# Optimization experiments

Measured on AMD Instinct MI355X. Metric: run time of the kernel, lower is better.

## Reference

```python
import jax, jax.numpy as jnp
import numpy as np

BATCH = 4096
DIM = 2048
TEMPERATURE = 0.5


def setup_inputs() -> dict:
    key = jax.random.key(0)
    k1, k2 = jax.random.split(key)
    c_i = jax.random.normal(k1, (BATCH, DIM), dtype=jnp.float32)
    c_j = jax.random.normal(k2, (BATCH, DIM), dtype=jnp.float32)
    return {"c_i": c_i, "c_j": c_j}


def reference(c_i, c_j):
    # Original torch loop computes, for each i,j:
    #   kl[i, j] = sum_k softmax(c_j[j])_k * (log_softmax(c_j[j])_k - log_softmax(c_i[i])_k)
    #   logits = -kl / T ; loss = CE(logits, arange(B), reduction='sum') / B
    # Fused: kl = hneg[None, :] - Li @ Q.T where hneg[j] = sum_k Q[j]*logQ[j].
    B = c_i.shape[0]
    Li = jax.nn.log_softmax(c_i, axis=-1)          # [B, D]
    LQ = jax.nn.log_softmax(c_j, axis=-1)          # [B, D]
    Q = jnp.exp(LQ)                                # softmax(c_j)
    hneg = jnp.sum(Q * LQ, axis=-1)                # [B] negative entropy of each c_j row
    cross = jnp.einsum("id,jd->ij", Li, Q)         # [B, B] sum_k Li[i,k]*Q[j,k]
    kl = hneg[None, :] - cross                     # [B, B]
    logits = -kl / TEMPERATURE
    logp = jax.nn.log_softmax(logits, axis=-1)     # [B, B]
    loss = -jnp.sum(jnp.diagonal(logp)) / B        # CE(sum) / batch_size
    return loss
```

## Files before the change

kernel.cpp:

```cpp
#include <hip/hip_runtime.h>
#include <hip/hip_bf16.h>
#include <math.h>

#define BATCH 4096
#define DIM   2048
#define INV_T 2.0f

#define BM 256
#define BN 256

typedef float floatx4 __attribute__((ext_vector_type(4)));
typedef int   intx4   __attribute__((ext_vector_type(4)));
typedef int   intx8   __attribute__((ext_vector_type(8)));

static __device__ __forceinline__ void gld_lds16(const void* g, void* l) {
  __builtin_amdgcn_global_load_lds(
      (const __attribute__((address_space(1))) void*)g,
      (__attribute__((address_space(3))) void*)l, 16, 0, 0);
}

static __device__ __forceinline__ intx8 comb8(intx4 lo, intx4 hi) {
  intx8 r;
  r[0] = lo[0]; r[1] = lo[1]; r[2] = lo[2]; r[3] = lo[3];
  r[4] = hi[0]; r[5] = hi[1]; r[6] = hi[2]; r[7] = hi[3];
  return r;
}

__global__ __launch_bounds__(256) void prep_kernel(
    const float* __restrict__ ci, const float* __restrict__ cj,
    unsigned char* __restrict__ Li8, unsigned char* __restrict__ Qb8,
    float* __restrict__ hneg, float* __restrict__ isc,
    float* __restrict__ rowsum, unsigned* __restrict__ cnt)
{
  const int lane = threadIdx.x & 63;
  const int wave = threadIdx.x >> 6;
  const int row = blockIdx.x * 4 + wave;
  const bool isj = row >= BATCH;
  const int r = isj ? row - BATCH : row;
  const float* __restrict__ src = (isj ? cj : ci) + (size_t)r * DIM;

  float v[32];
  #pragma unroll
  for (int i = 0; i < 8; ++i) {
    float4 t = ((const float4*)src)[i * 64 + lane];
    v[i * 4 + 0] = t.x; v[i * 4 + 1] = t.y;
    v[i * 4 + 2] = t.z; v[i * 4 + 3] = t.w;
  }

  float m = v[0];
  #pragma unroll
  for (int i = 1; i < 32; ++i) m = fmaxf(m, v[i]);
  #pragma unroll
  for (int off = 32; off >= 1; off >>= 1) m = fmaxf(m, __shfl_xor(m, off));

  float e[32];
  float s = 0.f;
  #pragma unroll
  for (int i = 0; i < 32; ++i) { e[i] = __expf(v[i] - m); s += e[i]; }
  #pragma unroll
  for (int off = 32; off >= 1; off >>= 1) s += __shfl_xor(s, off);
  const float ls = m + __logf(s);
  const float inv_s = 1.0f / s;

  float scale = 1.f;
  int t = 0;
  if (isj) {
    const int be = (int)((__float_as_uint(inv_s) >> 23) & 0xff);
    t = 134 - be;
    scale = __uint_as_float((unsigned)(t + 127) << 23);
  }

  unsigned char* dst = (isj ? Qb8 : Li8) + (size_t)r * DIM;
  float h = 0.f;
  #pragma unroll
  for (int i = 0; i < 8; ++i) {
    float f[4];
    #pragma unroll
    for (int j = 0; j < 4; ++j) {
      const float li = v[i * 4 + j] - ls;
      if (isj) {
        const float q = e[i * 4 + j] * inv_s;
        h += q * li;
        f[j] = q * scale;
      } else {
        f[j] = li;
      }
    }
    int w = __builtin_amdgcn_cvt_pk_fp8_f32(f[0], f[1], 0, false);
    w = __builtin_amdgcn_cvt_pk_fp8_f32(f[2], f[3], w, true);
    ((int*)dst)[i * 64 + lane] = w;
  }

  if (isj) {
    #pragma unroll
    for (int off = 32; off >= 1; off >>= 1) h += __shfl_xor(h, off);
    if (lane == 0) {
      hneg[r] = h;
      isc[r] = __uint_as_float((unsigned)(127 - t) << 23);
      rowsum[r] = 0.f;
    }
  }
  if (row == 0 && lane == 0) cnt[0] = 0u;
}

__global__ __launch_bounds__(512, 1) void gemm_lse_kernel(
    const unsigned char* __restrict__ Li8, const unsigned char* __restrict__ Qb8,
    const float* __restrict__ hneg, const float* __restrict__ isc,
    float* __restrict__ rowsum, float* __restrict__ diag,
    unsigned* __restrict__ cnt, float* __restrict__ out)
{
  __shared__ __attribute__((aligned(16))) unsigned char As_[2][BM * 128];
  __shared__ __attribute__((aligned(16))) unsigned char Bs_[2][BN * 128];

  const int tid  = threadIdx.x;
  const int lin = blockIdx.x;
  const int xc  = lin & 7;
  const int sq  = lin >> 3;
  const int by  = (xc & 3) * 4 + (sq & 3);
  const int bx  = (xc >> 2) * 8 + (sq >> 2);

  const int lane = tid & 63;
  const int wave = tid >> 6;
  const int wm   = wave >> 2;
  const int wn   = wave & 3;

  int soff[4];
  #pragma unroll
  for (int s = 0; s < 4; ++s) {
    const int p = tid + 512 * s;
    const int row = p >> 3;
    const int cbg = (p & 7) ^ (row & 7);
    soff[s] = row * DIM + cbg * 16;
  }
  const unsigned char* Abase = Li8 + (size_t)(by * BM) * DIM;
  const unsigned char* Bbase = Qb8 + (size_t)(bx * BN) * DIM;

  const int rl = lane & 15;
  const int q  = lane >> 4;
  const int sw = rl & 7;

  floatx4 acc[8][4];
  const floatx4 z = {0.f, 0.f, 0.f, 0.f};
  #pragma unroll
  for (int mt = 0; mt < 8; ++mt)
    #pragma unroll
    for (int nt = 0; nt < 4; ++nt) acc[mt][nt] = z;

  #pragma unroll
  for (int s = 0; s < 4; ++s) {
    gld_lds16(Abase + soff[s], &As_[0][0] + (tid + 512 * s) * 16);
    gld_lds16(Bbase + soff[s], &Bs_[0][0] + (tid + 512 * s) * 16);
  }

  for (int t = 0; t < 16; ++t) {
    const int cur = t & 1;
    const unsigned char* Ab = &As_[cur][0];
    const unsigned char* Bb = &Bs_[cur][0];

    if (t < 15) {
      unsigned char* An = &As_[cur ^ 1][0];
      unsigned char* Bn = &Bs_[cur ^ 1][0];
      const int kn = (t + 1) * 128;
      #pragma unroll
      for (int s = 0; s < 4; ++s) {
        gld_lds16(Abase + soff[s] + kn, An + (tid + 512 * s) * 16);
        gld_lds16(Bbase + soff[s] + kn, Bn + (tid + 512 * s) * 16);
      }
      asm volatile("s_waitcnt vmcnt(8)" ::: "memory");
    } else {
      asm volatile("s_waitcnt vmcnt(0)" ::: "memory");
    }
    asm volatile("s_barrier" ::: "memory");

    intx8 bf[4];
    #pragma unroll
    for (int nt = 0; nt < 4; ++nt) {
      const int rb = wn * 64 + nt * 16 + rl;
      const int q0 = rb * 8 + ((2 * q) ^ sw);
      const int q1 = rb * 8 + ((2 * q + 1) ^ sw);
      bf[nt] = comb8(*(const intx4*)(Bb + q0 * 16),
                     *(const intx4*)(Bb + q1 * 16));
    }
    intx8 af[2];
    {
      const int ra = wm * 128 + rl;
      const int a0 = ra * 8 + ((2 * q) ^ sw);
      const int a1 = ra * 8 + ((2 * q + 1) ^ sw);
      af[0] = comb8(*(const intx4*)(Ab + a0 * 16),
                    *(const intx4*)(Ab + a1 * 16));
    }
    #pragma unroll
    for (int s = 0; s < 8; ++s) {
      if (s < 7) {
        const int ra = wm * 128 + (s + 1) * 16 + rl;
        const int a0 = ra * 8 + ((2 * q) ^ sw);
        const int a1 = ra * 8 + ((2 * q + 1) ^ sw);
        af[(s + 1) & 1] = comb8(*(const intx4*)(Ab + a0 * 16),
                                *(const intx4*)(Ab + a1 * 16));
      }
      __builtin_amdgcn_s_setprio(1);
      #pragma unroll
      for (int nt = 0; nt < 4; ++nt)
        acc[s][nt] = __builtin_amdgcn_mfma_scale_f32_16x16x128_f8f6f4(
            af[s & 1], bf[nt], acc[s][nt],
            0, 0,
            0, 127,
            0, 127);
      __builtin_amdgcn_s_setprio(0);
    }

    asm volatile("s_barrier" ::: "memory");
  }

  const int col0 = bx * BN + wn * 64 + rl;
  float hn[4], sc[4];
  #pragma unroll
  for (int nt = 0; nt < 4; ++nt) {
    hn[nt] = hneg[col0 + nt * 16];
    sc[nt] = isc[col0 + nt * 16];
  }
  const int row0 = by * BM + wm * 128 + (q << 2);

  if (bx == by && wm == (wn >> 1) && q == (rl >> 2)) {
    #pragma unroll
    for (int half = 0; half < 2; ++half) {
      #pragma unroll
      for (int nt = 0; nt < 4; ++nt) {
        #pragma unroll
        for (int rr = 0; rr < 4; ++rr) {
          if ((wn & 1) == half && (rl & 3) == rr)
            atomicExch(&diag[bx * BN + wn * 64 + nt * 16 + rl],
                       acc[half * 4 + nt][nt][rr] * sc[nt]);
        }
      }
    }
  }

  #pragma unroll
  for (int mt = 0; mt < 8; ++mt) {
    #pragma unroll
    for (int rr = 0; rr < 4; ++rr) {
      float p = 0.f;
      #pragma unroll
      for (int nt = 0; nt < 4; ++nt)
        p += __expf(INV_T * (acc[mt][nt][rr] * sc[nt] - hn[nt]));
      p += __shfl_xor(p, 1);
      p += __shfl_xor(p, 2);
      p += __shfl_xor(p, 4);
      p += __shfl_xor(p, 8);
      if (rl == 0)
        atomicAdd(&rowsum[row0 + mt * 16 + rr], p);
    }
  }

  __shared__ unsigned last_flag;
  __syncthreads();
  if (tid == 0) {
    __threadfence();
    last_flag = (atomicAdd(cnt, 1u) == 255u);
  }
  __syncthreads();
  if (last_flag) {
    float c = 0.f;
    #pragma unroll
    for (int j = 0; j < 8; ++j) {
      const int i = tid + j * 512;
      c += __logf(rowsum[i]) - INV_T * (diag[i] - hneg[i]);
    }
    #pragma unroll
    for (int off = 32; off >= 1; off >>= 1) c += __shfl_xor(c, off);
    __shared__ float red[8];
    if (lane == 0) red[wave] = c;
    __syncthreads();
    if (tid == 0) {
      float tot = 0.f;
      #pragma unroll
      for (int w = 0; w < 8; ++w) tot += red[w];
      out[0] = tot * (1.0f / BATCH);
    }
  }
}

extern "C" void kernel_launch(void* const* d_in, const int* in_sizes, int n_in,
                              void* d_out, int out_size, void* d_ws, size_t ws_size,
                              hipStream_t stream) {
  const float* ci = (const float*)d_in[0];
  const float* cj = (const float*)d_in[1];
  float* out = (float*)d_out;

  unsigned char* Li8 = (unsigned char*)d_ws;
  unsigned char* Qb8 = Li8 + (size_t)BATCH * DIM;
  float* hneg   = (float*)(Qb8 + (size_t)BATCH * DIM);
  float* isc    = hneg + BATCH;
  float* rowsum = isc + BATCH;
  float* diag   = rowsum + BATCH;
  unsigned* cnt = (unsigned*)(diag + BATCH);

  prep_kernel<<<2 * BATCH / 4, 256, 0, stream>>>(ci, cj, Li8, Qb8, hneg, isc, rowsum, cnt);
  gemm_lse_kernel<<<(BATCH / BM) * (BATCH / BN), 512, 0, stream>>>(
      Li8, Qb8, hneg, isc, rowsum, diag, cnt, out);
}
```

Measured before the change: 143.3 us.

## Shrink GEMM tiles to 128x128 with 256-thread blocks, two blocks per CU

Reduces the block tile from 256x256 to 128x128 and moves to 4 waves per block, each computing a 64x64 subtile, with launch bounds allowing two blocks per CU. The grid becomes 1024 blocks with a new block-to-tile mapping, and the last-block reduction counter and final sum are adjusted to match. The aim is better occupancy and load balance across CUs, and latency hiding between co-resident blocks. The cost is lower reuse per loaded byte, which roughly doubles global/LDS traffic per FLOP, plus twice as many atomic row-sum updates.

```diff
diff --git a/kernel.cpp b/kernel.cpp
--- a/kernel.cpp
+++ b/kernel.cpp
@@ -6,8 +6,8 @@
 #define DIM   2048
 #define INV_T 2.0f
 
-#define BM 256
-#define BN 256
+#define BM 128
+#define BN 128
 
 typedef float floatx4 __attribute__((ext_vector_type(4)));
 typedef int   intx4   __attribute__((ext_vector_type(4)));
@@ -103,7 +103,7 @@
   if (row == 0 && lane == 0) cnt[0] = 0u;
 }
 
-__global__ __launch_bounds__(512, 1) void gemm_lse_kernel(
+__global__ __launch_bounds__(256, 2) void gemm_lse_kernel(
     const unsigned char* __restrict__ Li8, const unsigned char* __restrict__ Qb8,
     const float* __restrict__ hneg, const float* __restrict__ isc,
     float* __restrict__ rowsum, float* __restrict__ diag,
@@ -116,18 +116,18 @@
   const int lin = blockIdx.x;
   const int xc  = lin & 7;
   const int sq  = lin >> 3;
-  const int by  = (xc & 3) * 4 + (sq & 3);
-  const int bx  = (xc >> 2) * 8 + (sq >> 2);
+  const int by  = sq & 31;
+  const int bx  = xc * 4 + (sq >> 5);
 
   const int lane = tid & 63;
   const int wave = tid >> 6;
-  const int wm   = wave >> 2;
-  const int wn   = wave & 3;
+  const int ww   = wave >> 1;
+  const int wc   = wave & 1;
 
   int soff[4];
   #pragma unroll
   for (int s = 0; s < 4; ++s) {
-    const int p = tid + 512 * s;
+    const int p = tid + 256 * s;
     const int row = p >> 3;
     const int cbg = (p & 7) ^ (row & 7);
     soff[s] = row * DIM + cbg * 16;
@@ -139,17 +139,17 @@
   const int q  = lane >> 4;
   const int sw = rl & 7;
 
-  floatx4 acc[8][4];
+  floatx4 acc[4][4];
   const floatx4 z = {0.f, 0.f, 0.f, 0.f};
   #pragma unroll
-  for (int mt = 0; mt < 8; ++mt)
+  for (int mt = 0; mt < 4; ++mt)
     #pragma unroll
     for (int nt = 0; nt < 4; ++nt) acc[mt][nt] = z;
 
   #pragma unroll
   for (int s = 0; s < 4; ++s) {
-    gld_lds16(Abase + soff[s], &As_[0][0] + (tid + 512 * s) * 16);
-    gld_lds16(Bbase + soff[s], &Bs_[0][0] + (tid + 512 * s) * 16);
+    gld_lds16(Abase + soff[s], &As_[0][0] + (tid + 256 * s) * 16);
+    gld_lds16(Bbase + soff[s], &Bs_[0][0] + (tid + 256 * s) * 16);
   }
 
   for (int t = 0; t < 16; ++t) {
@@ -163,8 +163,8 @@
       const int kn = (t + 1) * 128;
       #pragma unroll
       for (int s = 0; s < 4; ++s) {
-        gld_lds16(Abase + soff[s] + kn, An + (tid + 512 * s) * 16);
-        gld_lds16(Bbase + soff[s] + kn, Bn + (tid + 512 * s) * 16);
+        gld_lds16(Abase + soff[s] + kn, An + (tid + 256 * s) * 16);
+        gld_lds16(Bbase + soff[s] + kn, Bn + (tid + 256 * s) * 16);
       }
       asm volatile("s_waitcnt vmcnt(8)" ::: "memory");
     } else {
@@ -172,72 +172,58 @@
     }
     asm volatile("s_barrier" ::: "memory");
 
-    intx8 bf[4];
-    #pragma unroll
-    for (int nt = 0; nt < 4; ++nt) {
-      const int rb = wn * 64 + nt * 16 + rl;
-      const int q0 = rb * 8 + ((2 * q) ^ sw);
-      const int q1 = rb * 8 + ((2 * q + 1) ^ sw);
-      bf[nt] = comb8(*(const intx4*)(Bb + q0 * 16),
-                     *(const intx4*)(Bb + q1 * 16));
-    }
-    intx8 af[2];
-    {
-      const int ra = wm * 128 + rl;
+    intx8 af[4], bf[4];
+    #pragma unroll
+    for (int i = 0; i < 4; ++i) {
+      const int ra = ww * 64 + i * 16 + rl;
       const int a0 = ra * 8 + ((2 * q) ^ sw);
       const int a1 = ra * 8 + ((2 * q + 1) ^ sw);
-      af[0] = comb8(*(const intx4*)(Ab + a0 * 16),
+      af[i] = comb8(*(const intx4*)(Ab + a0 * 16),
                     *(const intx4*)(Ab + a1 * 16));
-    }
-    #pragma unroll
-    for (int s = 0; s < 8; ++s) {
-      if (s < 7) {
-        const int ra = wm * 128 + (s + 1) * 16 + rl;
-        const int a0 = ra * 8 + ((2 * q) ^ sw);
-        const int a1 = ra * 8 + ((2 * q + 1) ^ sw);
-        af[(s + 1) & 1] = comb8(*(const intx4*)(Ab + a0 * 16),
-                                *(const intx4*)(Ab + a1 * 16));
-      }
-      __builtin_amdgcn_s_setprio(1);
+      const int rb = wc * 64 + i * 16 + rl;
+      const int b0 = rb * 8 + ((2 * q) ^ sw);
+      const int b1 = rb * 8 + ((2 * q + 1) ^ sw);
+      bf[i] = comb8(*(const intx4*)(Bb + b0 * 16),
+                    *(const intx4*)(Bb + b1 * 16));
+    }
+    __builtin_amdgcn_s_setprio(1);
+    #pragma unroll
+    for (int mt = 0; mt < 4; ++mt)
       #pragma unroll
       for (int nt = 0; nt < 4; ++nt)
-        acc[s][nt] = __builtin_amdgcn_mfma_scale_f32_16x16x128_f8f6f4(
-            af[s & 1], bf[nt], acc[s][nt],
+        acc[mt][nt] = __builtin_amdgcn_mfma_scale_f32_16x16x128_f8f6f4(
+            af[mt], bf[nt], acc[mt][nt],
             0, 0,
             0, 127,
             0, 127);
-      __builtin_amdgcn_s_setprio(0);
-    }
+    __builtin_amdgcn_s_setprio(0);
 
     asm volatile("s_barrier" ::: "memory");
   }
 
-  const int col0 = bx * BN + wn * 64 + rl;
+  const int col0 = bx * BN + wc * 64 + rl;
   float hn[4], sc[4];
   #pragma unroll
   for (int nt = 0; nt < 4; ++nt) {
     hn[nt] = hneg[col0 + nt * 16];
     sc[nt] = isc[col0 + nt * 16];
   }
-  const int row0 = by * BM + wm * 128 + (q << 2);
-
-  if (bx == by && wm == (wn >> 1) && q == (rl >> 2)) {
-    #pragma unroll
-    for (int half = 0; half < 2; ++half) {
-      #pragma unroll
-      for (int nt = 0; nt < 4; ++nt) {
-        #pragma unroll
-        for (int rr = 0; rr < 4; ++rr) {
-          if ((wn & 1) == half && (rl & 3) == rr)
-            atomicExch(&diag[bx * BN + wn * 64 + nt * 16 + rl],
-                       acc[half * 4 + nt][nt][rr] * sc[nt]);
-        }
+  const int row0 = by * BM + ww * 64 + (q << 2);
+
+  if (bx == by && ww == wc && q == (rl >> 2)) {
+    #pragma unroll
+    for (int nt = 0; nt < 4; ++nt) {
+      #pragma unroll
+      for (int rr = 0; rr < 4; ++rr) {
+        if ((rl & 3) == rr)
+          atomicExch(&diag[bx * BN + wc * 64 + nt * 16 + rl],
+                     acc[nt][nt][rr] * sc[nt]);
       }
     }
   }
 
   #pragma unroll
-  for (int mt = 0; mt < 8; ++mt) {
+  for (int mt = 0; mt < 4; ++mt) {
     #pragma unroll
     for (int rr = 0; rr < 4; ++rr) {
       float p = 0.f;
@@ -257,27 +243,23 @@
   __syncthreads();
   if (tid == 0) {
     __threadfence();
-    last_flag = (atomicAdd(cnt, 1u) == 255u);
+    last_flag = (atomicAdd(cnt, 1u) == 1023u);
   }
   __syncthreads();
   if (last_flag) {
     float c = 0.f;
     #pragma unroll
-    for (int j = 0; j < 8; ++j) {
-      const int i = tid + j * 512;
+    for (int j = 0; j < 16; ++j) {
+      const int i = tid + j * 256;
       c += __logf(rowsum[i]) - INV_T * (diag[i] - hneg[i]);
     }
     #pragma unroll
     for (int off = 32; off >= 1; off >>= 1) c += __shfl_xor(c, off);
-    __shared__ float red[8];
+    __shared__ float red[4];
     if (lane == 0) red[wave] = c;
     __syncthreads();
-    if (tid == 0) {
-      float tot = 0.f;
-      #pragma unroll
-      for (int w = 0; w < 8; ++w) tot += red[w];
-      out[0] = tot * (1.0f / BATCH);
-    }
+    if (tid == 0)
+      out[0] = (red[0] + red[1] + red[2] + red[3]) * (1.0f / BATCH);
   }
 }
 
@@ -297,6 +279,6 @@
   unsigned* cnt = (unsigned*)(diag + BATCH);
 
   prep_kernel<<<2 * BATCH / 4, 256, 0, stream>>>(ci, cj, Li8, Qb8, hneg, isc, rowsum, cnt);
-  gemm_lse_kernel<<<(BATCH / BM) * (BATCH / BN), 512, 0, stream>>>(
+  gemm_lse_kernel<<<(BATCH / BM) * (BATCH / BN), 256, 0, stream>>>(
       Li8, Qb8, hneg, isc, rowsum, diag, cnt, out);
 }
```

Result: slower. 152.4 us (+6.3%).
